# Optimization experiments

Measured on AMD Instinct MI355X. Metric: run time of the kernel, lower is better.

## Reference

```python
import jax, jax.numpy as jnp
import numpy as np

B, C, Q = 16, 1024, 128
XD, YD = 64, 32
D, H, HID, L = 512, 8, 2048, 6
HD = D // H
NEG = -1e9


def setup_inputs() -> dict:
    key = jax.random.key(0)
    ks = jax.random.split(key, 12)
    rn = lambda k, shape, s: jax.random.normal(k, shape, jnp.float32) * s
    return {
        "x_c": rn(ks[0], (B, C, XD), 1.0),
        "y_c": rn(ks[1], (B, C, YD), 1.0),
        "x_q": rn(ks[2], (B, Q, XD), 1.0),
        "W_val": rn(ks[3], (XD + YD, D), (XD + YD) ** -0.5),
        "b_val": jnp.zeros((D,), jnp.float32),
        "q_emb": rn(ks[4], (D,), D ** -0.5),
        "in_proj_w": rn(ks[5], (L, 3 * D, D), D ** -0.5),
        "in_proj_b": jnp.zeros((L, 3 * D), jnp.float32),
        "out_w": rn(ks[6], (L, D, D), D ** -0.5),
        "out_b": jnp.zeros((L, D), jnp.float32),
        "ln1_g": jnp.ones((L, D), jnp.float32),
        "ln1_b": jnp.zeros((L, D), jnp.float32),
        "lin1_w": rn(ks[7], (L, HID, D), D ** -0.5),
        "lin1_b": jnp.zeros((L, HID), jnp.float32),
        "lin2_w": rn(ks[8], (L, D, HID), HID ** -0.5),
        "lin2_b": jnp.zeros((L, D), jnp.float32),
        "ln2_g": jnp.ones((L, D), jnp.float32),
        "ln2_b": jnp.zeros((L, D), jnp.float32),
        "W_head": rn(ks[9], (D, YD), D ** -0.5),
        "b_head": jnp.zeros((YD,), jnp.float32),
    }


def _layernorm(x, g, b):
    mu = x.mean(-1, keepdims=True)
    var = ((x - mu) ** 2).mean(-1, keepdims=True)
    return (x - mu) * jax.lax.rsqrt(var + 1e-5) * g + b


def _forward(x_c, y_c, x_q, W_val, b_val, q_emb, in_proj_w, in_proj_b, out_w,
             out_b, ln1_g, ln1_b, lin1_w, lin1_b, lin2_w, lin2_b, ln2_g, ln2_b,
             W_head, b_head):
    bsz, c_len, _ = x_c.shape
    q_len = x_q.shape[1]
    S = c_len + q_len
    # concat y onto x; queries get zero y placeholder
    xy_c = jnp.concatenate([x_c, y_c], axis=-1)
    xy_q = jnp.concatenate([x_q, jnp.zeros((bsz, q_len, y_c.shape[-1]), x_q.dtype)], axis=-1)
    xy = jnp.concatenate([xy_c, xy_q], axis=1) @ W_val + b_val          # [B,S,D]
    xy = xy.at[:, -q_len:].add(q_emb)
    # src_mask: no one may attend to query positions (last q_len keys)
    bias = jnp.where(jnp.arange(S) >= c_len, jnp.float32(NEG), jnp.float32(0.0))  # [S] key axis

    def layer(x, p):
        ipw, ipb, ow, ob, g1, b1, w1, bb1, w2, bb2, g2, b2 = p
        qkv = x @ ipw.T + ipb                                           # [B,S,3D]
        q, k, v = jnp.split(qkv, 3, axis=-1)
        heads = lambda t: t.reshape(bsz, S, H, HD).transpose(0, 2, 1, 3)  # [B,H,S,HD]
        q, k, v = heads(q), heads(k), heads(v)
        scores = jnp.einsum('bhqd,bhkd->bhqk', q, k) / np.float32(np.sqrt(HD)) + bias
        attn = jax.nn.softmax(scores, axis=-1)
        ctx = jnp.einsum('bhqk,bhkd->bhqd', attn, v)
        ctx = ctx.transpose(0, 2, 1, 3).reshape(bsz, S, D)
        x = _layernorm(x + ctx @ ow.T + ob, g1, b1)                     # post-norm
        ff = jax.nn.relu(x @ w1.T + bb1) @ w2.T + bb2
        x = _layernorm(x + ff, g2, b2)
        return x, None

    params = (in_proj_w, in_proj_b, out_w, out_b, ln1_g, ln1_b,
              lin1_w, lin1_b, lin2_w, lin2_b, ln2_g, ln2_b)
    x, _ = jax.lax.scan(layer, xy, params)
    return x[:, -q_len:] @ W_head + b_head                              # [B,Q,YD]


def reference(x_c, y_c, x_q, W_val, b_val, q_emb, in_proj_w, in_proj_b, out_w,
              out_b, ln1_g, ln1_b, lin1_w, lin1_b, lin2_w, lin2_b, ln2_g, ln2_b,
              W_head, b_head):
    return _forward(x_c, y_c, x_q, W_val, b_val, q_emb, in_proj_w, in_proj_b,
                    out_w, out_b, ln1_g, ln1_b, lin1_w, lin1_b, lin2_w, lin2_b,
                    ln2_g, ln2_b, W_head, b_head)
```

## Files before the change

kernel.cpp:

```cpp
#include <hip/hip_runtime.h>

#define B_   16
#define C_   1024
#define Q_   128
#define S_   1152
#define D_   512
#define H_   8
#define HID_ 2048
#define L_   6
#define M_   (B_*S_)
#define MQ_  (B_*Q_)
#define QSC_ 0.18033688011f

typedef short bf16x8 __attribute__((ext_vector_type(8)));
typedef float f32x4  __attribute__((ext_vector_type(4)));
#define MFMA16(a,b,c) __builtin_amdgcn_mfma_f32_16x16x32_bf16(a,b,c,0,0,0)

__device__ __forceinline__ unsigned short f2b(float f){
  union { float f; unsigned u; } v; v.f = f;
  return (unsigned short)((v.u + 0x7FFF + ((v.u >> 16) & 1)) >> 16);
}
__device__ __forceinline__ void gload16(const void* g, void* l){
  __builtin_amdgcn_global_load_lds((const __attribute__((address_space(1))) void*)g,
                                   (__attribute__((address_space(3))) void*)l, 16, 0, 0);
}
__device__ __forceinline__ float waveSum(float v){
  #pragma unroll
  for (int o = 32; o > 0; o >>= 1) v += __shfl_down(v, o, 64);
  return v;
}

__global__ __launch_bounds__(256) void f2b_kernel(
    const float* __restrict__ in, unsigned short* __restrict__ out, int n4)
{
  int i = blockIdx.x*256 + threadIdx.x;
  for (; i < n4; i += gridDim.x*256) {
    float4 v = ((const float4*)in)[i];
    ushort4 o = { f2b(v.x), f2b(v.y), f2b(v.z), f2b(v.w) };
    ((ushort4*)out)[i] = o;
  }
}

__global__ __launch_bounds__(256) void f2bq_kernel(
    const float* __restrict__ in, unsigned short* __restrict__ out, int n4)
{
  int i = blockIdx.x*256 + threadIdx.x;
  for (; i < n4; i += gridDim.x*256) {
    const int row = (i >> 7) % 1536;
    const float s = (row < 512) ? QSC_ : 1.f;
    float4 v = ((const float4*)in)[i];
    ushort4 o = { f2b(v.x*s), f2b(v.y*s), f2b(v.z*s), f2b(v.w*s) };
    ((ushort4*)out)[i] = o;
  }
}

__global__ __launch_bounds__(256) void sbias_kernel(
    const float* __restrict__ in, float* __restrict__ out)
{
  int idx = blockIdx.x*256 + threadIdx.x;
  if (idx < L_*1536) {
    int j = idx % 1536;
    out[idx] = in[idx] * (j < 512 ? QSC_ : 1.f);
  }
}

__global__ __launch_bounds__(256) void packxy_kernel(
    const float* __restrict__ x_c, const float* __restrict__ y_c,
    const float* __restrict__ x_q, unsigned short* __restrict__ XY)
{
  int idx = blockIdx.x*256 + threadIdx.x;
  const int n = M_*128;
  for (; idx < n; idx += gridDim.x*256) {
    int row = idx >> 7, col = idx & 127;
    int bb = row / S_, s = row % S_;
    float v;
    if (col < 64) {
      v = (s < C_) ? x_c[((size_t)bb*C_ + s)*64 + col]
                   : x_q[((size_t)bb*Q_ + (s - C_))*64 + col];
    } else if (col < 96) {
      v = (s < C_) ? y_c[((size_t)bb*C_ + s)*32 + (col - 64)] : 0.f;
    } else if (col == 96) {
      v = 1.f;
    } else if (col == 97) {
      v = (s >= C_) ? 1.f : 0.f;
    } else v = 0.f;
    XY[idx] = f2b(v);
  }
}

__global__ __launch_bounds__(256) void wemb_kernel(
    const float* __restrict__ W_val, const float* __restrict__ b_val,
    const float* __restrict__ q_emb, unsigned short* __restrict__ Wemb)
{
  int idx = blockIdx.x*256 + threadIdx.x;
  int nn = idx >> 7, k = idx & 127;
  float v;
  if (k < 96)       v = W_val[k*D_ + nn];
  else if (k == 96) v = b_val[nn];
  else if (k == 97) v = q_emb[nn];
  else              v = 0.f;
  Wemb[idx] = f2b(v);
}

__global__ __launch_bounds__(256) void gatherq_kernel(
    const float* __restrict__ X, float* __restrict__ Xq)
{
  int row = blockIdx.x;
  int bb = row >> 7, qi = row & 127;
  const float* src = X + ((size_t)bb*S_ + C_ + qi)*D_;
  float* dst = Xq + (size_t)row*D_;
  int tid = threadIdx.x;
  dst[tid] = src[tid];
  dst[tid + 256] = src[tid + 256];
}

template<int RELU, int RES, int BOUT>
__global__ __launch_bounds__(256) void bgemm_kernel(
    const unsigned short* __restrict__ A, const unsigned short* __restrict__ W,
    const float* __restrict__ bias, const float* __restrict__ Rsd,
    float* __restrict__ Cf, unsigned short* __restrict__ Cb, int Nn, int Kk)
{
  __shared__ short As[2][4096];
  __shared__ short Bs[2][4096];
  int lin = blockIdx.y * gridDim.x + blockIdx.x;
  const int nwg = gridDim.x * gridDim.y;
  const int cpx = nwg >> 3;
  lin = (lin & 7) * cpx + (lin >> 3);
  const int bm = (lin / gridDim.x) * 128, bn = (lin % gridDim.x) * 128;

  const int tid = threadIdx.x;
  const int w = tid >> 6, lane = tid & 63, l15 = lane & 15, l4 = lane >> 4;
  const int wm = w >> 1, wn = w & 1;
  f32x4 acc[4][4] = {};
  const size_t strA = (size_t)Kk * 2;
  const char* Abase = (const char*)A + (size_t)bm * strA;
  const char* Wbase = (const char*)W + (size_t)bn * strA;
  const size_t soff = (size_t)(tid >> 2) * strA + (size_t)((tid & 3) * 16);
  const int ldsOff = w * 1024;

#define STAGEK(K0, BUF) do { \
    const char* a0_ = Abase + soff + (size_t)(K0)*2; \
    const char* b0_ = Wbase + soff + (size_t)(K0)*2; \
    char* la_ = (char*)As + (BUF)*8192 + ldsOff; \
    char* lb_ = (char*)Bs + (BUF)*8192 + ldsOff; \
    gload16(a0_,            la_); \
    gload16(a0_ + 64*strA,  la_ + 4096); \
    gload16(b0_,            lb_); \
    gload16(b0_ + 64*strA,  lb_ + 4096); \
  } while(0)

  STAGEK(0, 0);
  const int nk = Kk >> 5;
  for (int t = 0; t < nk; t++) {
    __syncthreads();
    if (t + 1 < nk) STAGEK((t+1)*32, (t+1)&1);
    const short* AsC = (const short*)As + (t&1)*4096;
    const short* BsC = (const short*)Bs + (t&1)*4096;
    bf16x8 af[4], bfr[4];
    #pragma unroll
    for (int mf = 0; mf < 4; mf++)
      af[mf] = *(const bf16x8*)(AsC + (wm*64 + mf*16 + l15)*32 + l4*8);
    #pragma unroll
    for (int nf = 0; nf < 4; nf++)
      bfr[nf] = *(const bf16x8*)(BsC + (wn*64 + nf*16 + l15)*32 + l4*8);
    #pragma unroll
    for (int mf = 0; mf < 4; mf++)
      #pragma unroll
      for (int nf = 0; nf < 4; nf++)
        acc[mf][nf] = MFMA16(af[mf], bfr[nf], acc[mf][nf]);
  }
#undef STAGEK

  #pragma unroll
  for (int mf = 0; mf < 4; mf++) {
    #pragma unroll
    for (int nf = 0; nf < 4; nf++) {
      const int ccol = bn + wn*64 + nf*16 + l15;
      const float bv = bias[ccol];
      #pragma unroll
      for (int r = 0; r < 4; r++) {
        const int rrow = bm + wm*64 + mf*16 + l4*4 + r;
        float o = acc[mf][nf][r] + bv;
        if (RELU) o = fmaxf(o, 0.f);
        if (RES)  o += Rsd[(size_t)rrow*Nn + ccol];
        if (BOUT == 1)      Cb[(size_t)rrow*Nn + ccol] = f2b(o);
        else if (BOUT == 0) Cf[(size_t)rrow*Nn + ccol] = o;
        else { Cf[(size_t)rrow*Nn + ccol] = o; Cb[(size_t)rrow*Nn + ccol] = f2b(o); }
      }
    }
  }
}

template<int RELU, int RES, int BOUT>
__global__ __launch_bounds__(256) void bgemm64_kernel(
    const unsigned short* __restrict__ A, const unsigned short* __restrict__ W,
    const float* __restrict__ bias, const float* __restrict__ Rsd,
    float* __restrict__ Cf, unsigned short* __restrict__ Cb, int Nn, int Kk)
{
  __shared__ short As[2][4096];
  __shared__ short Bs[2][2048];
  int lin = blockIdx.y * gridDim.x + blockIdx.x;
  const int nwg = gridDim.x * gridDim.y;
  const int cpx = nwg >> 3;
  lin = (lin & 7) * cpx + (lin >> 3);
  const int bm = (lin / gridDim.x) * 128, bn = (lin % gridDim.x) * 64;

  const int tid = threadIdx.x;
  const int w = tid >> 6, lane = tid & 63, l15 = lane & 15, l4 = lane >> 4;
  f32x4 acc[2][4] = {};
  const size_t strA = (size_t)Kk * 2;
  const char* Abase = (const char*)A + (size_t)bm * strA;
  const char* Wbase = (const char*)W + (size_t)bn * strA;
  const size_t soff = (size_t)(tid >> 2) * strA + (size_t)((tid & 3) * 16);
  const int ldsOff = w * 1024;

#define STAGEK64(K0, BUF) do { \
    const char* a0_ = Abase + soff + (size_t)(K0)*2; \
    const char* b0_ = Wbase + soff + (size_t)(K0)*2; \
    char* la_ = (char*)As + (BUF)*8192 + ldsOff; \
    char* lb_ = (char*)Bs + (BUF)*4096 + ldsOff; \
    gload16(a0_,            la_); \
    gload16(a0_ + 64*strA,  la_ + 4096); \
    gload16(b0_,            lb_); \
  } while(0)

  STAGEK64(0, 0);
  const int nk = Kk >> 5;
  for (int t = 0; t < nk; t++) {
    __syncthreads();
    if (t + 1 < nk) STAGEK64((t+1)*32, (t+1)&1);
    const short* AsC = (const short*)As + (t&1)*4096;
    const short* BsC = (const short*)Bs + (t&1)*2048;
    bf16x8 af[2], bfr[4];
    #pragma unroll
    for (int mf = 0; mf < 2; mf++)
      af[mf] = *(const bf16x8*)(AsC + (w*32 + mf*16 + l15)*32 + l4*8);
    #pragma unroll
    for (int nf = 0; nf < 4; nf++)
      bfr[nf] = *(const bf16x8*)(BsC + (nf*16 + l15)*32 + l4*8);
    #pragma unroll
    for (int mf = 0; mf < 2; mf++)
      #pragma unroll
      for (int nf = 0; nf < 4; nf++)
        acc[mf][nf] = MFMA16(af[mf], bfr[nf], acc[mf][nf]);
  }
#undef STAGEK64

  #pragma unroll
  for (int mf = 0; mf < 2; mf++) {
    #pragma unroll
    for (int nf = 0; nf < 4; nf++) {
      const int ccol = bn + nf*16 + l15;
      const float bv = bias[ccol];
      #pragma unroll
      for (int r = 0; r < 4; r++) {
        const int rrow = bm + w*32 + mf*16 + l4*4 + r;
        float o = acc[mf][nf][r] + bv;
        if (RELU) o = fmaxf(o, 0.f);
        if (RES)  o += Rsd[(size_t)rrow*Nn + ccol];
        if (BOUT == 1)      Cb[(size_t)rrow*Nn + ccol] = f2b(o);
        else if (BOUT == 0) Cf[(size_t)rrow*Nn + ccol] = o;
        else { Cf[(size_t)rrow*Nn + ccol] = o; Cb[(size_t)rrow*Nn + ccol] = f2b(o); }
      }
    }
  }
}

__global__ __launch_bounds__(256) void mattn_kernel(
    const unsigned short* __restrict__ QKV, unsigned short* __restrict__ Ctx,
    int nqt, int qoff, int orows)
{
  __shared__ short Ks[64*72];
  __shared__ short Vt[64*72];
  __shared__ short Ps[4*16*72];
  const int bid = blockIdx.x;
  const int qt = bid % nqt;
  const int h  = (bid / nqt) % H_;
  const int bb = bid / (nqt*H_);
  const int tid = threadIdx.x;
  const int w = tid >> 6, lane = tid & 63, l15 = lane & 15, l4 = lane >> 4;

  const size_t rowQ = (size_t)bb*S_ + qoff + (size_t)qt*64 + w*16 + l15;
  const unsigned short* qp = QKV + rowQ*1536 + h*64;
  const bf16x8 qf0 = *(const bf16x8*)(qp + l4*8);
  const bf16x8 qf1 = *(const bf16x8*)(qp + 32 + l4*8);

  const unsigned short* Kg = QKV + (size_t)bb*S_*1536 + 512 + h*64;
  const unsigned short* Vg = Kg + 512;

  f32x4 ctx[4] = {};
  f32x4 lacc = {};
  float m_r[4];
  #pragma unroll
  for (int r = 0; r < 4; r++) m_r[r] = -3.0e38f;

  const bf16x8 onesv = {(short)0x3F80,(short)0x3F80,(short)0x3F80,(short)0x3F80,
                        (short)0x3F80,(short)0x3F80,(short)0x3F80,(short)0x3F80};

  char* PsW = (char*)Ps + w*2304;

  const int skey = tid >> 3, shc = tid & 7;
  const int vp   = tid >> 3, vhc = tid & 7;

  const unsigned short* gK = Kg + (size_t)skey*1536 + shc*8;
  const unsigned short* gV = Vg + (size_t)(2*vp)*1536 + vhc*8;
  bf16x8 k0v = *(const bf16x8*)gK;
  bf16x8 k1v = *(const bf16x8*)(gK + 32*1536);
  bf16x8 c0  = *(const bf16x8*)gV;
  bf16x8 c1  = *(const bf16x8*)(gV + 1536);

  for (int kt = 0; kt < 16; kt++) {
    __syncthreads();
    *(bf16x8*)((char*)Ks + skey*144      + shc*16) = k0v;
    *(bf16x8*)((char*)Ks + (skey+32)*144 + shc*16) = k1v;
    #pragma unroll
    for (int j = 0; j < 8; j++) {
      const int hd = vhc*8 + j;
      unsigned int val = (unsigned int)(unsigned short)c0[j]
                       | ((unsigned int)(unsigned short)c1[j] << 16);
      *(unsigned int*)((char*)Vt + hd*144 + ((4*vp) ^ (vhc<<4))) = val;
    }
    __syncthreads();
    if (kt < 15) {
      const unsigned short* nK = gK + (size_t)(kt+1)*98304;
      const unsigned short* nV = gV + (size_t)(kt+1)*98304;
      k0v = *(const bf16x8*)nK;
      k1v = *(const bf16x8*)(nK + 32*1536);
      c0  = *(const bf16x8*)nV;
      c1  = *(const bf16x8*)(nV + 1536);
    }

    f32x4 sac[4] = {};
    __builtin_amdgcn_s_setprio(1);
    #pragma unroll
    for (int nf = 0; nf < 4; nf++) {
      const char* kb = (char*)Ks + (nf*16 + l15)*144 + l4*16;
      bf16x8 b0 = *(const bf16x8*)kb;
      bf16x8 b1 = *(const bf16x8*)(kb + 64);
      sac[nf] = MFMA16(qf0, b0, sac[nf]);
      sac[nf] = MFMA16(qf1, b1, sac[nf]);
    }
    __builtin_amdgcn_s_setprio(0);

    float lmax[4];
    #pragma unroll
    for (int r = 0; r < 4; r++)
      lmax[r] = fmaxf(fmaxf(sac[0][r], sac[1][r]), fmaxf(sac[2][r], sac[3][r]));
    int ok = 1;
    #pragma unroll
    for (int r = 0; r < 4; r++) ok &= (lmax[r] <= m_r[r] + 11.5409f) ? 1 : 0;
    if (!__all(ok)) {
      #pragma unroll
      for (int r = 0; r < 4; r++) {
        float t = lmax[r];
        t = fmaxf(t, __shfl_xor(t, 1, 64));
        t = fmaxf(t, __shfl_xor(t, 2, 64));
        t = fmaxf(t, __shfl_xor(t, 4, 64));
        t = fmaxf(t, __shfl_xor(t, 8, 64));
        const float mn = fmaxf(m_r[r], t);
        const float scl = __builtin_amdgcn_exp2f(m_r[r] - mn);
        m_r[r] = mn;
        lacc[r] *= scl;
        ctx[0][r] *= scl; ctx[1][r] *= scl;
        ctx[2][r] *= scl; ctx[3][r] *= scl;
      }
    }
    #pragma unroll
    for (int r = 0; r < 4; r++) {
      unsigned short* pw = (unsigned short*)(PsW + (l4*4 + r)*144);
      const float m0 = m_r[r];
      pw[ 0 + l15] = (unsigned short)(__float_as_uint(__builtin_amdgcn_exp2f(sac[0][r] - m0)) >> 16);
      pw[16 + l15] = (unsigned short)(__float_as_uint(__builtin_amdgcn_exp2f(sac[1][r] - m0)) >> 16);
      pw[32 + l15] = (unsigned short)(__float_as_uint(__builtin_amdgcn_exp2f(sac[2][r] - m0)) >> 16);
      pw[48 + l15] = (unsigned short)(__float_as_uint(__builtin_amdgcn_exp2f(sac[3][r] - m0)) >> 16);
    }

    const char* pb = PsW + l15*144 + l4*16;
    const bf16x8 pf0 = *(const bf16x8*)pb;
    const bf16x8 pf1 = *(const bf16x8*)(pb + 64);
    __builtin_amdgcn_s_setprio(1);
    lacc = MFMA16(pf0, onesv, lacc);
    lacc = MFMA16(pf1, onesv, lacc);
    #pragma unroll
    for (int hf = 0; hf < 4; hf++) {
      const int hd = hf*16 + l15;
      const int hc = (hd >> 3) & 7;
      const char* vb = (char*)Vt + hd*144;
      bf16x8 v0 = *(const bf16x8*)(vb + ((l4*16)     ^ (hc<<4)));
      bf16x8 v1 = *(const bf16x8*)(vb + (((l4+4)*16) ^ (hc<<4)));
      ctx[hf] = MFMA16(pf0, v0, ctx[hf]);
      ctx[hf] = MFMA16(pf1, v1, ctx[hf]);
    }
    __builtin_amdgcn_s_setprio(0);
  }

  #pragma unroll
  for (int r = 0; r < 4; r++) {
    const float invl = 1.0f / lacc[r];
    const size_t row = (size_t)bb*orows + (size_t)qt*64 + w*16 + l4*4 + r;
    unsigned short* op = Ctx + row*512 + h*64;
    op[ 0 + l15] = f2b(ctx[0][r]*invl);
    op[16 + l15] = f2b(ctx[1][r]*invl);
    op[32 + l15] = f2b(ctx[2][r]*invl);
    op[48 + l15] = f2b(ctx[3][r]*invl);
  }
}

__global__ __launch_bounds__(256) void ln_kernel(
    const float* __restrict__ Yin, const float* __restrict__ g, const float* __restrict__ b,
    float* __restrict__ Xf, unsigned short* __restrict__ Xb)
{
  int row = blockIdx.x, tid = threadIdx.x;
  const float* yr = Yin + (size_t)row*D_;
  float v0 = yr[tid], v1 = yr[tid + 256];
  __shared__ float red[4];
  float s = waveSum(v0 + v1);
  if ((tid & 63) == 0) red[tid >> 6] = s;
  __syncthreads();
  float mu = (red[0] + red[1] + red[2] + red[3]) * (1.f/512.f);
  __syncthreads();
  float d0 = v0 - mu, d1 = v1 - mu;
  float ss = waveSum(d0*d0 + d1*d1);
  if ((tid & 63) == 0) red[tid >> 6] = ss;
  __syncthreads();
  float inv = rsqrtf((red[0] + red[1] + red[2] + red[3]) * (1.f/512.f) + 1e-5f);
  float o0 = d0 * inv * g[tid]       + b[tid];
  float o1 = d1 * inv * g[tid + 256] + b[tid + 256];
  Xf[(size_t)row*D_ + tid]       = o0;
  Xf[(size_t)row*D_ + tid + 256] = o1;
  Xb[(size_t)row*D_ + tid]       = f2b(o0);
  Xb[(size_t)row*D_ + tid + 256] = f2b(o1);
}

__global__ __launch_bounds__(64) void head_kernel(
    const float* __restrict__ Xq, const float* __restrict__ W_head,
    const float* __restrict__ b_head, float* __restrict__ out)
{
  int row = blockIdx.x;
  const float* xr = Xq + (size_t)row*D_;
  __shared__ float xs[512];
  int tid = threadIdx.x;
  for (int i = tid; i < 512; i += 64) xs[i] = xr[i];
  __syncthreads();
  if (tid < 32) {
    float acc = b_head[tid];
    #pragma unroll 8
    for (int k = 0; k < 512; k++) acc += xs[k] * W_head[k*32 + tid];
    out[(size_t)row*32 + tid] = acc;
  }
}

extern "C" void kernel_launch(void* const* d_in, const int* in_sizes, int n_in,
                              void* d_out, int out_size, void* d_ws, size_t ws_size,
                              hipStream_t stream)
{
  const float* x_c      = (const float*)d_in[0];
  const float* y_c      = (const float*)d_in[1];
  const float* x_q      = (const float*)d_in[2];
  const float* W_val    = (const float*)d_in[3];
  const float* b_val    = (const float*)d_in[4];
  const float* q_emb    = (const float*)d_in[5];
  const float* in_proj_w= (const float*)d_in[6];
  const float* in_proj_b= (const float*)d_in[7];
  const float* out_w    = (const float*)d_in[8];
  const float* out_b    = (const float*)d_in[9];
  const float* ln1_g    = (const float*)d_in[10];
  const float* ln1_b    = (const float*)d_in[11];
  const float* lin1_w   = (const float*)d_in[12];
  const float* lin1_b   = (const float*)d_in[13];
  const float* lin2_w   = (const float*)d_in[14];
  const float* lin2_b   = (const float*)d_in[15];
  const float* ln2_g    = (const float*)d_in[16];
  const float* ln2_b    = (const float*)d_in[17];
  const float* W_head   = (const float*)d_in[18];
  const float* b_head   = (const float*)d_in[19];
  float* out = (float*)d_out;

  char* p = (char*)d_ws;
  float* X = (float*)p;                 p += (size_t)M_*D_*4;
  char*  YH = p;                        p += (size_t)M_*HID_*2;
  float* Y = (float*)YH;
  unsigned short* hid = (unsigned short*)YH;
  unsigned short* Xb   = (unsigned short*)p; p += (size_t)M_*D_*2;
  unsigned short* qkv  = (unsigned short*)p; p += (size_t)M_*3*D_*2;
  unsigned short* ctxb = (unsigned short*)p; p += (size_t)M_*D_*2;
  unsigned short* ipwB = (unsigned short*)p; p += (size_t)L_*3*D_*D_*2;
  unsigned short* owB  = (unsigned short*)p; p += (size_t)L_*D_*D_*2;
  unsigned short* w1B  = (unsigned short*)p; p += (size_t)L_*HID_*D_*2;
  unsigned short* w2B  = (unsigned short*)p; p += (size_t)L_*D_*HID_*2;
  unsigned short* XYb  = (unsigned short*)p; p += (size_t)M_*128*2;
  unsigned short* Wemb = (unsigned short*)p; p += (size_t)D_*128*2;
  float* zbias         = (float*)p;          p += 2048*4;
  float* qkvbias       = (float*)p;          p += L_*1536*4;

  unsigned short* ctxq = ctxb;
  float*          Yq   = (float*)YH;
  unsigned short* hidq = (unsigned short*)(YH + (size_t)16*1024*1024);
  float*          Xq   = (float*)XYb;
  unsigned short* Xqb  = (unsigned short*)((char*)XYb + (size_t)MQ_*D_*4);

  (void)hipMemsetAsync(zbias, 0, 2048*4, stream);

  f2bq_kernel<<<512, 256, 0, stream>>>(in_proj_w, ipwB, L_*3*D_*D_/4);
  sbias_kernel<<<36, 256, 0, stream>>>(in_proj_b, qkvbias);
  f2b_kernel<<<512, 256, 0, stream>>>(out_w,     owB,  L_*D_*D_/4);
  f2b_kernel<<<512, 256, 0, stream>>>(lin1_w,    w1B,  L_*HID_*D_/4);
  f2b_kernel<<<512, 256, 0, stream>>>(lin2_w,    w2B,  L_*D_*HID_/4);
  wemb_kernel<<<256, 256, 0, stream>>>(W_val, b_val, q_emb, Wemb);
  packxy_kernel<<<1024, 256, 0, stream>>>(x_c, y_c, x_q, XYb);

  bgemm_kernel<0,0,2><<<dim3(4, 144), 256, 0, stream>>>(
      XYb, Wemb, zbias, nullptr, X, Xb, D_, 128);

  for (int l = 0; l < L_ - 1; l++) {
    bgemm_kernel<0,0,1><<<dim3(12, 144), 256, 0, stream>>>(
        Xb, ipwB + (size_t)l*3*D_*D_, qkvbias + (size_t)l*3*D_,
        nullptr, nullptr, qkv, 3*D_, D_);
    mattn_kernel<<<B_*H_*18, 256, 0, stream>>>(qkv, ctxb, 18, 0, S_);
    bgemm64_kernel<0,1,0><<<dim3(8, 144), 256, 0, stream>>>(
        ctxb, owB + (size_t)l*D_*D_, out_b + (size_t)l*D_,
        X, Y, nullptr, D_, D_);
    ln_kernel<<<M_, 256, 0, stream>>>(Y, ln1_g + (size_t)l*D_, ln1_b + (size_t)l*D_, X, Xb);
    bgemm_kernel<1,0,1><<<dim3(16, 144), 256, 0, stream>>>(
        Xb, w1B + (size_t)l*HID_*D_, lin1_b + (size_t)l*HID_,
        nullptr, nullptr, hid, HID_, D_);
    bgemm64_kernel<0,1,0><<<dim3(8, 144), 256, 0, stream>>>(
        hid, w2B + (size_t)l*D_*HID_, lin2_b + (size_t)l*D_,
        X, X, nullptr, D_, HID_);
    ln_kernel<<<M_, 256, 0, stream>>>(X, ln2_g + (size_t)l*D_, ln2_b + (size_t)l*D_, X, Xb);
  }

  {
    const int l = L_ - 1;
    bgemm_kernel<0,0,1><<<dim3(12, 144), 256, 0, stream>>>(
        Xb, ipwB + (size_t)l*3*D_*D_, qkvbias + (size_t)l*3*D_,
        nullptr, nullptr, qkv, 3*D_, D_);
    mattn_kernel<<<B_*H_*2, 256, 0, stream>>>(qkv, ctxq, 2, C_, Q_);
    gatherq_kernel<<<MQ_, 256, 0, stream>>>(X, Xq);
    bgemm64_kernel<0,1,0><<<dim3(8, 16), 256, 0, stream>>>(
        ctxq, owB + (size_t)l*D_*D_, out_b + (size_t)l*D_,
        Xq, Yq, nullptr, D_, D_);
    ln_kernel<<<MQ_, 256, 0, stream>>>(Yq, ln1_g + (size_t)l*D_, ln1_b + (size_t)l*D_, Xq, Xqb);
    bgemm_kernel<1,0,1><<<dim3(16, 16), 256, 0, stream>>>(
        Xqb, w1B + (size_t)l*HID_*D_, lin1_b + (size_t)l*HID_,
        nullptr, nullptr, hidq, HID_, D_);
    bgemm64_kernel<0,1,0><<<dim3(8, 16), 256, 0, stream>>>(
        hidq, w2B + (size_t)l*D_*HID_, lin2_b + (size_t)l*D_,
        Xq, Xq, nullptr, D_, HID_);
    ln_kernel<<<MQ_, 256, 0, stream>>>(Xq, ln2_g + (size_t)l*D_, ln2_b + (size_t)l*D_, Xq, Xqb);
  }

  head_kernel<<<MQ_, 64, 0, stream>>>(Xq, W_head, b_head, out);
}
```

Before: 1.826 ms.

## Drop fp32 residual stream, keep activations in bf16 only; swizzle attention blocks

The fp32 copy of the hidden state is removed. Residual adds now read the bf16 activation buffer, and layernorm writes only bf16 output, which cuts fp32 writes and reads per layer. The qkv buffer is reused to hold the post-LN1 activations, and the last-layer gather and head now work on bf16. The attention kernel also gets an XCD-style block-index swizzle. The cost is lower residual precision, since the residual is now rounded to bf16 at every layer.

Result: faster. 1.765 ms (-3.3%).

```diff
diff --git a/kernel.cpp b/kernel.cpp
--- a/kernel.cpp
+++ b/kernel.cpp
@@ -19,6 +19,9 @@
 __device__ __forceinline__ unsigned short f2b(float f){
   union { float f; unsigned u; } v; v.f = f;
   return (unsigned short)((v.u + 0x7FFF + ((v.u >> 16) & 1)) >> 16);
+}
+__device__ __forceinline__ float b2f(unsigned short u){
+  return __uint_as_float((unsigned)u << 16);
 }
 __device__ __forceinline__ void gload16(const void* g, void* l){
   __builtin_amdgcn_global_load_lds((const __attribute__((address_space(1))) void*)g,
@@ -103,21 +106,21 @@
 }
 
 __global__ __launch_bounds__(256) void gatherq_kernel(
-    const float* __restrict__ X, float* __restrict__ Xq)
+    const unsigned short* __restrict__ X, unsigned short* __restrict__ Xq)
 {
   int row = blockIdx.x;
   int bb = row >> 7, qi = row & 127;
-  const float* src = X + ((size_t)bb*S_ + C_ + qi)*D_;
-  float* dst = Xq + (size_t)row*D_;
+  const unsigned short* src = X + ((size_t)bb*S_ + C_ + qi)*D_;
+  unsigned short* dst = Xq + (size_t)row*D_;
   int tid = threadIdx.x;
   dst[tid] = src[tid];
   dst[tid + 256] = src[tid + 256];
 }
 
-template<int RELU, int RES, int BOUT>
+template<int RELU, int BOUT>
 __global__ __launch_bounds__(256) void bgemm_kernel(
     const unsigned short* __restrict__ A, const unsigned short* __restrict__ W,
-    const float* __restrict__ bias, const float* __restrict__ Rsd,
+    const float* __restrict__ bias,
     float* __restrict__ Cf, unsigned short* __restrict__ Cb, int Nn, int Kk)
 {
   __shared__ short As[2][4096];
@@ -182,20 +185,17 @@
         const int rrow = bm + wm*64 + mf*16 + l4*4 + r;
         float o = acc[mf][nf][r] + bv;
         if (RELU) o = fmaxf(o, 0.f);
-        if (RES)  o += Rsd[(size_t)rrow*Nn + ccol];
-        if (BOUT == 1)      Cb[(size_t)rrow*Nn + ccol] = f2b(o);
-        else if (BOUT == 0) Cf[(size_t)rrow*Nn + ccol] = o;
-        else { Cf[(size_t)rrow*Nn + ccol] = o; Cb[(size_t)rrow*Nn + ccol] = f2b(o); }
+        if (BOUT == 1) Cb[(size_t)rrow*Nn + ccol] = f2b(o);
+        else           Cf[(size_t)rrow*Nn + ccol] = o;
       }
     }
   }
 }
 
-template<int RELU, int RES, int BOUT>
 __global__ __launch_bounds__(256) void bgemm64_kernel(
     const unsigned short* __restrict__ A, const unsigned short* __restrict__ W,
-    const float* __restrict__ bias, const float* __restrict__ Rsd,
-    float* __restrict__ Cf, unsigned short* __restrict__ Cb, int Nn, int Kk)
+    const float* __restrict__ bias, const unsigned short* __restrict__ Rsd,
+    float* __restrict__ Cf, int Nn, int Kk)
 {
   __shared__ short As[2][4096];
   __shared__ short Bs[2][2048];
@@ -255,12 +255,8 @@
       #pragma unroll
       for (int r = 0; r < 4; r++) {
         const int rrow = bm + w*32 + mf*16 + l4*4 + r;
-        float o = acc[mf][nf][r] + bv;
-        if (RELU) o = fmaxf(o, 0.f);
-        if (RES)  o += Rsd[(size_t)rrow*Nn + ccol];
-        if (BOUT == 1)      Cb[(size_t)rrow*Nn + ccol] = f2b(o);
-        else if (BOUT == 0) Cf[(size_t)rrow*Nn + ccol] = o;
-        else { Cf[(size_t)rrow*Nn + ccol] = o; Cb[(size_t)rrow*Nn + ccol] = f2b(o); }
+        float o = acc[mf][nf][r] + bv + b2f(Rsd[(size_t)rrow*Nn + ccol]);
+        Cf[(size_t)rrow*Nn + ccol] = o;
       }
     }
   }
@@ -273,7 +269,9 @@
   __shared__ short Ks[64*72];
   __shared__ short Vt[64*72];
   __shared__ short Ps[4*16*72];
-  const int bid = blockIdx.x;
+  int bid = blockIdx.x;
+  const int nwg = gridDim.x;
+  bid = (bid & 7) * (nwg >> 3) + (bid >> 3);
   const int qt = bid % nqt;
   const int h  = (bid / nqt) % H_;
   const int bb = bid / (nqt*H_);
@@ -408,7 +406,7 @@
 
 __global__ __launch_bounds__(256) void ln_kernel(
     const float* __restrict__ Yin, const float* __restrict__ g, const float* __restrict__ b,
-    float* __restrict__ Xf, unsigned short* __restrict__ Xb)
+    unsigned short* __restrict__ Xb)
 {
   int row = blockIdx.x, tid = threadIdx.x;
   const float* yr = Yin + (size_t)row*D_;
@@ -424,23 +422,19 @@
   if ((tid & 63) == 0) red[tid >> 6] = ss;
   __syncthreads();
   float inv = rsqrtf((red[0] + red[1] + red[2] + red[3]) * (1.f/512.f) + 1e-5f);
-  float o0 = d0 * inv * g[tid]       + b[tid];
-  float o1 = d1 * inv * g[tid + 256] + b[tid + 256];
-  Xf[(size_t)row*D_ + tid]       = o0;
-  Xf[(size_t)row*D_ + tid + 256] = o1;
-  Xb[(size_t)row*D_ + tid]       = f2b(o0);
-  Xb[(size_t)row*D_ + tid + 256] = f2b(o1);
+  Xb[(size_t)row*D_ + tid]       = f2b(d0 * inv * g[tid]       + b[tid]);
+  Xb[(size_t)row*D_ + tid + 256] = f2b(d1 * inv * g[tid + 256] + b[tid + 256]);
 }
 
 __global__ __launch_bounds__(64) void head_kernel(
-    const float* __restrict__ Xq, const float* __restrict__ W_head,
+    const unsigned short* __restrict__ Xq, const float* __restrict__ W_head,
     const float* __restrict__ b_head, float* __restrict__ out)
 {
   int row = blockIdx.x;
-  const float* xr = Xq + (size_t)row*D_;
+  const unsigned short* xr = Xq + (size_t)row*D_;
   __shared__ float xs[512];
   int tid = threadIdx.x;
-  for (int i = tid; i < 512; i += 64) xs[i] = xr[i];
+  for (int i = tid; i < 512; i += 64) xs[i] = b2f(xr[i]);
   __syncthreads();
   if (tid < 32) {
     float acc = b_head[tid];
@@ -477,12 +471,11 @@
   float* out = (float*)d_out;
 
   char* p = (char*)d_ws;
-  float* X = (float*)p;                 p += (size_t)M_*D_*4;
-  char*  YH = p;                        p += (size_t)M_*HID_*2;
-  float* Y = (float*)YH;
-  unsigned short* hid = (unsigned short*)YH;
-  unsigned short* Xb   = (unsigned short*)p; p += (size_t)M_*D_*2;
+  float* Yf = (float*)p;                     p += (size_t)M_*D_*4;
+  unsigned short* hid  = (unsigned short*)p; p += (size_t)M_*HID_*2;
+  unsigned short* Xb2  = (unsigned short*)p; p += (size_t)M_*D_*2;
   unsigned short* qkv  = (unsigned short*)p; p += (size_t)M_*3*D_*2;
+  unsigned short* Xb1  = qkv;
   unsigned short* ctxb = (unsigned short*)p; p += (size_t)M_*D_*2;
   unsigned short* ipwB = (unsigned short*)p; p += (size_t)L_*3*D_*D_*2;
   unsigned short* owB  = (unsigned short*)p; p += (size_t)L_*D_*D_*2;
@@ -493,11 +486,12 @@
   float* zbias         = (float*)p;          p += 2048*4;
   float* qkvbias       = (float*)p;          p += L_*1536*4;
 
-  unsigned short* ctxq = ctxb;
-  float*          Yq   = (float*)YH;
-  unsigned short* hidq = (unsigned short*)(YH + (size_t)16*1024*1024);
-  float*          Xq   = (float*)XYb;
-  unsigned short* Xqb  = (unsigned short*)((char*)XYb + (size_t)MQ_*D_*4);
+
+  unsigned short* ctxq  = ctxb;
+  float*          Yfq   = Yf;
+  unsigned short* hidq  = hid;
+  unsigned short* Xqb2  = XYb;
+  unsigned short* Xqb1  = XYb + (size_t)MQ_*D_;
 
   (void)hipMemsetAsync(zbias, 0, 2048*4, stream);
 
@@ -509,46 +503,42 @@
   wemb_kernel<<<256, 256, 0, stream>>>(W_val, b_val, q_emb, Wemb);
   packxy_kernel<<<1024, 256, 0, stream>>>(x_c, y_c, x_q, XYb);
 
-  bgemm_kernel<0,0,2><<<dim3(4, 144), 256, 0, stream>>>(
-      XYb, Wemb, zbias, nullptr, X, Xb, D_, 128);
+  bgemm_kernel<0,1><<<dim3(4, 144), 256, 0, stream>>>(
+      XYb, Wemb, zbias, nullptr, Xb2, D_, 128);
 
   for (int l = 0; l < L_ - 1; l++) {
-    bgemm_kernel<0,0,1><<<dim3(12, 144), 256, 0, stream>>>(
-        Xb, ipwB + (size_t)l*3*D_*D_, qkvbias + (size_t)l*3*D_,
-        nullptr, nullptr, qkv, 3*D_, D_);
+    bgemm_kernel<0,1><<<dim3(12, 144), 256, 0, stream>>>(
+        Xb2, ipwB + (size_t)l*3*D_*D_, qkvbias + (size_t)l*3*D_,
+        nullptr, qkv, 3*D_, D_);
     mattn_kernel<<<B_*H_*18, 256, 0, stream>>>(qkv, ctxb, 18, 0, S_);
-    bgemm64_kernel<0,1,0><<<dim3(8, 144), 256, 0, stream>>>(
-        ctxb, owB + (size_t)l*D_*D_, out_b + (size_t)l*D_,
-        X, Y, nullptr, D_, D_);
-    ln_kernel<<<M_, 256, 0, stream>>>(Y, ln1_g + (size_t)l*D_, ln1_b + (size_t)l*D_, X, Xb);
-    bgemm_kernel<1,0,1><<<dim3(16, 144), 256, 0, stream>>>(
-        Xb, w1B + (size_t)l*HID_*D_, lin1_b + (size_t)l*HID_,
-        nullptr, nullptr, hid, HID_, D_);
-    bgemm64_kernel<0,1,0><<<dim3(8, 144), 256, 0, stream>>>(
-        hid, w2B + (size_t)l*D_*HID_, lin2_b + (size_t)l*D_,
-        X, X, nullptr, D_, HID_);
-    ln_kernel<<<M_, 256, 0, stream>>>(X, ln2_g + (size_t)l*D_, ln2_b + (size_t)l*D_, X, Xb);
+    bgemm64_kernel<<<dim3(8, 144), 256, 0, stream>>>(
+        ctxb, owB + (size_t)l*D_*D_, out_b + (size_t)l*D_, Xb2, Yf, D_, D_);
+    ln_kernel<<<M_, 256, 0, stream>>>(Yf, ln1_g + (size_t)l*D_, ln1_b + (size_t)l*D_, Xb1);
+    bgemm_kernel<1,1><<<dim3(16, 144), 256, 0, stream>>>(
+        Xb1, w1B + (size_t)l*HID_*D_, lin1_b + (size_t)l*HID_,
+        nullptr, hid, HID_, D_);
+    bgemm64_kernel<<<dim3(8, 144), 256, 0, stream>>>(
+        hid, w2B + (size_t)l*D_*HID_, lin2_b + (size_t)l*D_, Xb1, Yf, D_, HID_);
+    ln_kernel<<<M_, 256, 0, stream>>>(Yf, ln2_g + (size_t)l*D_, ln2_b + (size_t)l*D_, Xb2);
   }
 
   {
     const int l = L_ - 1;
-    bgemm_kernel<0,0,1><<<dim3(12, 144), 256, 0, stream>>>(
-        Xb, ipwB + (size_t)l*3*D_*D_, qkvbias + (size_t)l*3*D_,
-        nullptr, nullptr, qkv, 3*D_, D_);
+    bgemm_kernel<0,1><<<dim3(12, 144), 256, 0, stream>>>(
+        Xb2, ipwB + (size_t)l*3*D_*D_, qkvbias + (size_t)l*3*D_,
+        nullptr, qkv, 3*D_, D_);
     mattn_kernel<<<B_*H_*2, 256, 0, stream>>>(qkv, ctxq, 2, C_, Q_);
-    gatherq_kernel<<<MQ_, 256, 0, stream>>>(X, Xq);
-    bgemm64_kernel<0,1,0><<<dim3(8, 16), 256, 0, stream>>>(
-        ctxq, owB + (size_t)l*D_*D_, out_b + (size_t)l*D_,
-        Xq, Yq, nullptr, D_, D_);
-    ln_kernel<<<MQ_, 256, 0, stream>>>(Yq, ln1_g + (size_t)l*D_, ln1_b + (size_t)l*D_, Xq, Xqb);
-    bgemm_kernel<1,0,1><<<dim3(16, 16), 256, 0, stream>>>(
-        Xqb, w1B + (size_t)l*HID_*D_, lin1_b + (size_t)l*HID_,
-        nullptr, nullptr, hidq, HID_, D_);
-    bgemm64_kernel<0,1,0><<<dim3(8, 16), 256, 0, stream>>>(
-        hidq, w2B + (size_t)l*D_*HID_, lin2_b + (size_t)l*D_,
-        Xq, Xq, nullptr, D_, HID_);
-    ln_kernel<<<MQ_, 256, 0, stream>>>(Xq, ln2_g + (size_t)l*D_, ln2_b + (size_t)l*D_, Xq, Xqb);
-  }
-
-  head_kernel<<<MQ_, 64, 0, stream>>>(Xq, W_head, b_head, out);
-}
+    gatherq_kernel<<<MQ_, 256, 0, stream>>>(Xb2, Xqb2);
+    bgemm64_kernel<<<dim3(8, 16), 256, 0, stream>>>(
+        ctxq, owB + (size_t)l*D_*D_, out_b + (size_t)l*D_, Xqb2, Yfq, D_, D_);
+    ln_kernel<<<MQ_, 256, 0, stream>>>(Yfq, ln1_g + (size_t)l*D_, ln1_b + (size_t)l*D_, Xqb1);
+    bgemm_kernel<1,1><<<dim3(16, 16), 256, 0, stream>>>(
+        Xqb1, w1B + (size_t)l*HID_*D_, lin1_b + (size_t)l*HID_,
+        nullptr, hidq, HID_, D_);
+    bgemm64_kernel<<<dim3(8, 16), 256, 0, stream>>>(
+        hidq, w2B + (size_t)l*D_*HID_, lin2_b + (size_t)l*D_, Xqb1, Yfq, D_, HID_);
+    ln_kernel<<<MQ_, 256, 0, stream>>>(Yfq, ln2_g + (size_t)l*D_, ln2_b + (size_t)l*D_, Xqb2);
+  }
+
+  head_kernel<<<MQ_, 64, 0, stream>>>(Xqb2, W_head, b_head, out);
+}
```
